# Kernel tuning notes

Measured on AMD Instinct MI355X. Metric: run time of the kernel, lower is better.

Reference implementation:

```python
import jax, jax.numpy as jnp
import numpy as np
import math

B, SQ, SKV = 8, 1024, 1024
D, H, DQ, DV = 1024, 16, 64, 64
EPS = 1e-3  # Keras LayerNormalization default epsilon
IN_DECODER = True


def _layer_norm(x, gamma, beta):
    m = jnp.mean(x, axis=-1, keepdims=True)
    v = jnp.mean((x - m) ** 2, axis=-1, keepdims=True)
    return gamma * (x - m) / jnp.sqrt(v + EPS) + beta


def setup_inputs() -> dict:
    key = jax.random.key(0)
    ks = jax.random.split(key, 6)
    x = jax.random.normal(ks[0], (B, SQ, D), dtype=jnp.float32)
    # self-attention: query and key/value sequences are the same tensor
    lengths = jax.random.randint(ks[1], (B,), SKV // 2, SKV + 1, dtype=jnp.int32)
    init = 0.02
    Wq = jax.random.normal(ks[2], (D, H * DQ), dtype=jnp.float32) * init
    Wkv = jax.random.normal(ks[3], (D, H * (DQ + DV)), dtype=jnp.float32) * init
    Wo = jax.random.normal(ks[4], (H * DV, D), dtype=jnp.float32) * init
    return {
        "query_sequences": x,
        "key_value_sequences": x,
        "key_value_sequence_lengths": lengths,
        "Wq": Wq, "bq": jnp.zeros((H * DQ,), jnp.float32),
        "Wkv": Wkv, "bkv": jnp.zeros((H * (DQ + DV),), jnp.float32),
        "Wo": Wo, "bo": jnp.zeros((D,), jnp.float32),
        "ln_gamma": jnp.ones((D,), jnp.float32),
        "ln_beta": jnp.zeros((D,), jnp.float32),
    }


def reference(query_sequences, key_value_sequences, key_value_sequence_lengths,
              Wq, bq, Wkv, bkv, Wo, bo, ln_gamma, ln_beta):
    # detect self-attention exactly as the original (elementwise equality)
    self_attn = jnp.all(query_sequences == key_value_sequences)
    q_seq = _layer_norm(query_sequences, ln_gamma, ln_beta)
    kv_ln = _layer_norm(key_value_sequences, ln_gamma, ln_beta)
    kv_seq = jnp.where(self_attn, kv_ln, key_value_sequences)
    residual = q_seq  # pre-norm residual (original adds post-LN queries)

    q = (q_seq @ Wq + bq).reshape(B, SQ, H, DQ).transpose(0, 2, 1, 3)   # b h q d
    kvp = kv_seq @ Wkv + bkv
    k = kvp[..., : H * DQ].reshape(B, SKV, H, DQ).transpose(0, 2, 1, 3)  # b h k d
    v = kvp[..., H * DQ:].reshape(B, SKV, H, DV).transpose(0, 2, 1, 3)   # b h k d

    scores = jnp.einsum("bhqd,bhkd->bhqk", q, k) / math.sqrt(DQ)
    # padding mask on keys
    not_pad = (jnp.arange(SKV)[None, None, None, :]
               < key_value_sequence_lengths[:, None, None, None])
    scores = jnp.where(not_pad, scores, -jnp.inf)
    if IN_DECODER:
        causal = jnp.tril(jnp.ones((SQ, SKV), dtype=bool))[None, None]
        scores = jnp.where(jnp.logical_or(~self_attn, causal), scores, -jnp.inf)

    attn = jax.nn.softmax(scores, axis=-1)  # dropout is identity in eval mode
    out = jnp.einsum("bhqk,bhkd->bhqd", attn, v)
    out = out.transpose(0, 2, 1, 3).reshape(B, SQ, H * DV)
    out = out @ Wo + bo
    return out + residual
```

## Files before the change

kernel.cpp:

```cpp
#include <hip/hip_runtime.h>

typedef unsigned short u16;
typedef unsigned int u32;
typedef __attribute__((ext_vector_type(8))) short short8;
typedef __attribute__((ext_vector_type(4))) float fx4;

#define LOG2E 1.44269504088896340736f

__device__ __forceinline__ u16 f2bf(float f) {
    unsigned int u = __float_as_uint(f);
    u += 0x7fffu + ((u >> 16) & 1u);
    return (u16)(u >> 16);
}

__device__ __forceinline__ float bf2f(u16 v) {
    u32 u = ((u32)v) << 16;
    return __uint_as_float(u);
}

__device__ __forceinline__ u32 pack_bf2(float lo, float hi) {
    return __builtin_amdgcn_perm(__float_as_uint(hi), __float_as_uint(lo), 0x07060302u);
}

__device__ __forceinline__ float fast_exp2(float x) {
#if __has_builtin(__builtin_amdgcn_exp2f)
    return __builtin_amdgcn_exp2f(x);
#else
    return exp2f(x);
#endif
}

__device__ __forceinline__ fx4 mfma16(short8 a, short8 b, fx4 c) {
    return __builtin_amdgcn_mfma_f32_16x16x32_bf16(a, b, c, 0, 0, 0);
}

__device__ __forceinline__ void gload_lds16(const u16* g, u16* l) {
    __builtin_amdgcn_global_load_lds(
        (const __attribute__((address_space(1))) void*)g,
        (__attribute__((address_space(3))) void*)l, 16, 0, 0);
}

__global__ __launch_bounds__(256) void ln_kernel(
    const float* __restrict__ x, const float* __restrict__ gamma,
    const float* __restrict__ beta, u16* __restrict__ yb) {
    int wave = threadIdx.x >> 6, lane = threadIdx.x & 63;
    int row = (blockIdx.x << 2) + wave;
    const float* xr = x + ((size_t)row << 10);
    float4 v[4];
    float s = 0.0f, sq = 0.0f;
#pragma unroll
    for (int i = 0; i < 4; ++i) {
        v[i] = *(const float4*)(xr + (i << 8) + (lane << 2));
        s  += v[i].x + v[i].y + v[i].z + v[i].w;
        sq += v[i].x * v[i].x + v[i].y * v[i].y + v[i].z * v[i].z + v[i].w * v[i].w;
    }
#pragma unroll
    for (int o = 32; o > 0; o >>= 1) {
        s  += __shfl_xor(s, o, 64);
        sq += __shfl_xor(sq, o, 64);
    }
    float mean = s * (1.0f / 1024.0f);
    float var  = sq * (1.0f / 1024.0f) - mean * mean;
    float rstd = rsqrtf(var + 1e-3f);
#pragma unroll
    for (int i = 0; i < 4; ++i) {
        int off = (i << 8) + (lane << 2);
        float4 g  = *(const float4*)(gamma + off);
        float4 bb = *(const float4*)(beta + off);
        float4 y;
        y.x = (v[i].x - mean) * rstd * g.x + bb.x;
        y.y = (v[i].y - mean) * rstd * g.y + bb.y;
        y.z = (v[i].z - mean) * rstd * g.z + bb.z;
        y.w = (v[i].w - mean) * rstd * g.w + bb.w;
        unsigned long long p = (unsigned long long)f2bf(y.x)
            | ((unsigned long long)f2bf(y.y) << 16)
            | ((unsigned long long)f2bf(y.z) << 32)
            | ((unsigned long long)f2bf(y.w) << 48);
        *(unsigned long long*)(yb + ((size_t)row << 10) + off) = p;
    }
}

__global__ __launch_bounds__(256) void wt_kernel(
    const float* __restrict__ Wq, const float* __restrict__ Wkv,
    const float* __restrict__ Wo, u16* __restrict__ Wt) {
    int n0 = blockIdx.x << 5;
    int k0 = blockIdx.y << 5;
    const float* W; int sn0, SN;
    if (n0 < 1024)      { W = Wq;  sn0 = n0;        SN = 1024; }
    else if (n0 < 3072) { W = Wkv; sn0 = n0 - 1024; SN = 2048; }
    else                { W = Wo;  sn0 = n0 - 3072; SN = 1024; }
    __shared__ float tile[32][33];
    int tx = threadIdx.x & 31, ty = threadIdx.x >> 5;
#pragma unroll
    for (int r = 0; r < 4; ++r)
        tile[ty + r * 8][tx] = W[(size_t)(k0 + ty + r * 8) * SN + sn0 + tx];
    __syncthreads();
#pragma unroll
    for (int r = 0; r < 4; ++r)
        Wt[(size_t)(n0 + ty + r * 8) * 1024 + k0 + tx] = f2bf(tile[tx][ty + r * 8]);
}

__global__ __launch_bounds__(256) void vtrans_kernel(
    const u16* __restrict__ QKVp, u16* __restrict__ Vt) {
    int bh = blockIdx.x;
    int b = bh >> 4, h = bh & 15;
    int kt = blockIdx.y;
    int t = threadIdx.x;
    __shared__ u16 tile[64][80];
    int seg = t & 7;
#pragma unroll
    for (int p = 0; p < 2; ++p) {
        int k = (t >> 3) + (p << 5);
        *(uint4*)&tile[k][seg << 3] =
            *(const uint4*)(QKVp + (size_t)((b << 10) + (kt << 6) + k) * 3072
                            + 2048 + (h << 6) + (seg << 3));
    }
    __syncthreads();
#pragma unroll
    for (int p = 0; p < 2; ++p) {
        int d = (t >> 3) + (p << 5);
        __align__(16) u16 vals[8];
#pragma unroll
        for (int e = 0; e < 8; ++e) {
            int kp = (seg << 3) + e;
            int ksrc = ((kp & 3) << 4) + (kp >> 2);
            vals[e] = tile[ksrc][d];
        }
        *(uint4*)(Vt + (size_t)((bh << 6) + d) * 1024 + (kt << 6) + (seg << 3)) =
            *(uint4*)vals;
    }
}

template <int MODE, int WMT>
__global__ __launch_bounds__(256) void gemm_bt(
    const u16* __restrict__ A, const u16* __restrict__ Bt,
    const float* __restrict__ bq, const float* __restrict__ bkv,
    const u16* __restrict__ resb, float* __restrict__ Cf, u16* __restrict__ Cb,
    int M, int N, int K, float qscale) {
    __shared__ __align__(16) u16 sA[WMT * 32 * 64];
    __shared__ __align__(16) u16 sB[128 * 64];
    int m0 = blockIdx.y * (WMT * 32), n0 = blockIdx.x << 7;
    int tid = threadIdx.x, lane = tid & 63, wave = tid >> 6;
    int quad = lane >> 4, l15 = lane & 15, swr = lane & 7;
    int wm = (wave >> 1) * (WMT * 16), wn = (wave & 1) << 6;
    int srow = lane >> 3;
    int gseg = (lane & 7) ^ srow;

    fx4 acc[WMT][4];
    fx4 zero = {0.0f, 0.0f, 0.0f, 0.0f};
#pragma unroll
    for (int i = 0; i < WMT; ++i)
#pragma unroll
        for (int j = 0; j < 4; ++j) acc[i][j] = zero;

    for (int k0 = 0; k0 < K; k0 += 64) {
#pragma unroll
        for (int t = 0; t < WMT; ++t) {
            int cA = wave * WMT + t;
            int rowA = (cA << 3) + srow;
            gload_lds16(A + (size_t)(m0 + rowA) * K + k0 + (gseg << 3), &sA[cA << 9]);
            if (t < 4) {
                int cB = (wave << 2) + t;
                int rowB = (cB << 3) + srow;
                gload_lds16(Bt + (size_t)(n0 + rowB) * K + k0 + (gseg << 3), &sB[cB << 9]);
            }
        }
        __syncthreads();
#pragma unroll
        for (int kk = 0; kk < 64; kk += 32) {
            int ks = (kk >> 3) + quad;
            short8 af[WMT], bf[4];
#pragma unroll
            for (int mt = 0; mt < WMT; ++mt) {
                int r = wm + (mt << 4) + l15;
                af[mt] = *(const short8*)&sA[(r << 6) + (((ks ^ swr) & 7) << 3)];
            }
#pragma unroll
            for (int nt = 0; nt < 4; ++nt) {
                int r = wn + (nt << 4) + l15;
                bf[nt] = *(const short8*)&sB[(r << 6) + (((ks ^ swr) & 7) << 3)];
            }
#pragma unroll
            for (int mt = 0; mt < WMT; ++mt)
#pragma unroll
                for (int nt = 0; nt < 4; ++nt)
                    acc[mt][nt] = mfma16(af[mt], bf[nt], acc[mt][nt]);
        }
        __syncthreads();
    }

#pragma unroll
    for (int mt = 0; mt < WMT; ++mt)
#pragma unroll
        for (int nt = 0; nt < 4; ++nt)
#pragma unroll
            for (int r = 0; r < 4; ++r) {
                int row = m0 + wm + (mt << 4) + (quad << 2) + r;
                int col = n0 + wn + (nt << 4) + l15;
                if (MODE == 1) {
                    float v = acc[mt][nt][r] + bq[col];
                    size_t idx = (size_t)row * N + col;
                    Cf[idx] = v + bf2f(resb[idx]);
                } else {
                    float bias = (col < 1024) ? bq[col] : bkv[col - 1024];
                    float v = acc[mt][nt][r] + bias;
                    if (col < 1024) v *= qscale;
                    Cb[(size_t)row * N + col] = f2bf(v);
                }
            }
}

__global__ __launch_bounds__(256) void attn_kernel(
    const u16* __restrict__ QKVp, const u16* __restrict__ Vt,
    const int* __restrict__ lens, u16* __restrict__ O) {
    int bh = blockIdx.x;
    int b = bh >> 4, h = bh & 15;
    int j = blockIdx.y;
    int len = lens[b];
    int cap = (len - 1) >> 6;
    int tid = threadIdx.x, lane = tid & 63, w = tid >> 6;
    int quad = lane >> 4, l15 = lane & 15;

    __shared__ __align__(16) u16 sK[64 * 64];
    __shared__ __align__(16) u16 sV[64 * 64];
    __shared__ __align__(16) u16 sP[4 * 2048];
    u16* sPw = &sP[w << 11];

    int lrow = lane >> 3;
    int lseg = lane & 7;

    fx4 zero = {0.0f, 0.0f, 0.0f, 0.0f};

#pragma unroll
    for (int phase = 0; phase < 2; ++phase) {
        int s = phase ? (7 - j) : j;
        int q0 = s << 7;
        int wq0 = q0 + (w << 5);
        int ktend_blk = min((q0 + 127) >> 6, cap);
        int ktend_w   = min((wq0 + 31) >> 6, cap);

        short8 qf[2][2];
#pragma unroll
        for (int mt = 0; mt < 2; ++mt)
#pragma unroll
            for (int kk = 0; kk < 2; ++kk) {
                int qrow = (b << 10) + wq0 + (mt << 4) + l15;
                qf[mt][kk] = *(const short8*)(QKVp + (size_t)qrow * 3072
                              + (h << 6) + (kk << 5) + (quad << 3));
            }

        fx4 oacc[2][4];
        float lsum[2][4];
#pragma unroll
        for (int mt = 0; mt < 2; ++mt)
#pragma unroll
            for (int nt = 0; nt < 4; ++nt) oacc[mt][nt] = zero;
#pragma unroll
        for (int mt = 0; mt < 2; ++mt)
#pragma unroll
            for (int r = 0; r < 4; ++r) lsum[mt][r] = 0.0f;

        for (int kt = 0; kt <= ktend_blk; ++kt) {
            int k0g = kt << 6;
#pragma unroll
            for (int i = 0; i < 2; ++i) {
                int row = (w << 4) + (i << 3) + lrow;
                int gs = lseg ^ (row & 7);
                gload_lds16(QKVp + (size_t)((b << 10) + k0g + row) * 3072
                               + 1024 + (h << 6) + (gs << 3),
                            &sK[((w << 1) + i) << 9]);
                gload_lds16(Vt + (size_t)((bh << 6) + row) * 1024
                               + k0g + (gs << 3),
                            &sV[((w << 1) + i) << 9]);
            }
            __syncthreads();

            if (kt <= ktend_w) {
                fx4 sacc[2][4];
#pragma unroll
                for (int mt = 0; mt < 2; ++mt)
#pragma unroll
                    for (int nt = 0; nt < 4; ++nt) sacc[mt][nt] = zero;
#pragma unroll
                for (int kk = 0; kk < 2; ++kk) {
                    int seg = (kk << 2) + quad;
                    short8 kf[4];
#pragma unroll
                    for (int nt = 0; nt < 4; ++nt) {
                        int row = (nt << 4) + l15;
                        kf[nt] = *(const short8*)&sK[(row << 6)
                                   + (((seg ^ (row & 7)) & 7) << 3)];
                    }
#pragma unroll
                    for (int mt = 0; mt < 2; ++mt)
#pragma unroll
                        for (int nt = 0; nt < 4; ++nt)
                            sacc[mt][nt] = mfma16(qf[mt][kk], kf[nt], sacc[mt][nt]);
                }

                bool needm = ((k0g + 63) > wq0) || ((k0g + 64) > len);
                if (needm) {
#pragma unroll
                    for (int mt = 0; mt < 2; ++mt)
#pragma unroll
                        for (int nt = 0; nt < 4; ++nt) {
                            int kg = k0g + (nt << 4) + l15;
#pragma unroll
                            for (int r = 0; r < 4; ++r) {
                                int qr = wq0 + (mt << 4) + (quad << 2) + r;
                                if (kg > qr || kg >= len)
                                    sacc[mt][nt][r] = -30000.0f;
                            }
                        }
                }

#pragma unroll
                for (int mt = 0; mt < 2; ++mt) {
#pragma unroll
                    for (int nt = 0; nt < 4; ++nt)
#pragma unroll
                        for (int r = 0; r < 4; ++r)
                            sacc[mt][nt][r] = fast_exp2(sacc[mt][nt][r]);
#pragma unroll
                    for (int r = 0; r < 4; ++r) {
                        lsum[mt][r] += (sacc[mt][0][r] + sacc[mt][1][r])
                                     + (sacc[mt][2][r] + sacc[mt][3][r]);
                        int row = (mt << 4) + (quad << 2) + r;
                        u32 lo = pack_bf2(sacc[mt][0][r], sacc[mt][1][r]);
                        u32 hi = pack_bf2(sacc[mt][2][r], sacc[mt][3][r]);
                        uint2 pv; pv.x = lo; pv.y = hi;
                        int addr = (row << 6)
                                 + (((((l15 >> 1)) ^ (row & 7)) & 7) << 3)
                                 + ((l15 & 1) << 2);
                        *(uint2*)&sPw[addr] = pv;
                    }
                }
                __builtin_amdgcn_s_waitcnt(0xC07F);

#pragma unroll
                for (int kk = 0; kk < 2; ++kk) {
                    int seg = (kk << 2) + quad;
                    short8 vf[4], pf[2];
#pragma unroll
                    for (int nt = 0; nt < 4; ++nt) {
                        int row = (nt << 4) + l15;
                        vf[nt] = *(const short8*)&sV[(row << 6)
                                   + (((seg ^ (row & 7)) & 7) << 3)];
                    }
#pragma unroll
                    for (int mt = 0; mt < 2; ++mt) {
                        int row = (mt << 4) + l15;
                        pf[mt] = *(const short8*)&sPw[(row << 6)
                                   + (((seg ^ (row & 7)) & 7) << 3)];
                    }
#pragma unroll
                    for (int mt = 0; mt < 2; ++mt)
#pragma unroll
                        for (int nt = 0; nt < 4; ++nt)
                            oacc[mt][nt] = mfma16(pf[mt], vf[nt], oacc[mt][nt]);
                }
            }
            __syncthreads();
        }

#pragma unroll
        for (int mt = 0; mt < 2; ++mt)
#pragma unroll
            for (int r = 0; r < 4; ++r) {
                float v = lsum[mt][r];
                v += __shfl_xor(v, 1, 64);
                v += __shfl_xor(v, 2, 64);
                v += __shfl_xor(v, 4, 64);
                v += __shfl_xor(v, 8, 64);
                lsum[mt][r] = __builtin_amdgcn_rcpf(v);
            }
#pragma unroll
        for (int mt = 0; mt < 2; ++mt)
#pragma unroll
            for (int nt = 0; nt < 4; ++nt)
#pragma unroll
                for (int r = 0; r < 4; ++r) {
                    int row = (b << 10) + wq0 + (mt << 4) + (quad << 2) + r;
                    int col = (h << 6) + (nt << 4) + l15;
                    O[((size_t)row << 10) + col] =
                        f2bf(oacc[mt][nt][r] * lsum[mt][r]);
                }
    }
}

extern "C" void kernel_launch(void* const* d_in, const int* in_sizes, int n_in,
                              void* d_out, int out_size, void* d_ws, size_t ws_size,
                              hipStream_t stream) {
    (void)in_sizes; (void)n_in; (void)out_size; (void)ws_size;
    const float* x    = (const float*)d_in[0];
    const int*   lens = (const int*)d_in[2];
    const float* Wq   = (const float*)d_in[3];
    const float* bq   = (const float*)d_in[4];
    const float* Wkv  = (const float*)d_in[5];
    const float* bkv  = (const float*)d_in[6];
    const float* Wo   = (const float*)d_in[7];
    const float* bo   = (const float*)d_in[8];
    const float* gam  = (const float*)d_in[9];
    const float* bet  = (const float*)d_in[10];
    float* out = (float*)d_out;

    char* w = (char*)d_ws;
    u16* xln_b  = (u16*)w;  w += (size_t)8192 * 1024 * 2;
    u16* Wall_t = (u16*)w;  w += (size_t)4096 * 1024 * 2;
    u16* QKVp   = (u16*)w;  w += (size_t)8192 * 3072 * 2;
    u16* Vt     = (u16*)w;  w += (size_t)8192 * 1024 * 2;
    u16* AO     = (u16*)w;  w += (size_t)8192 * 1024 * 2;

    ln_kernel<<<2048, 256, 0, stream>>>(x, gam, bet, xln_b);
    wt_kernel<<<dim3(128, 32), 256, 0, stream>>>(Wq, Wkv, Wo, Wall_t);
    gemm_bt<0, 8><<<dim3(24, 32), 256, 0, stream>>>(xln_b, Wall_t, bq, bkv,
        nullptr, nullptr, QKVp, 8192, 3072, 1024, 0.125f * LOG2E);
    vtrans_kernel<<<dim3(128, 16), 256, 0, stream>>>(QKVp, Vt);
    attn_kernel<<<dim3(128, 4), 256, 0, stream>>>(QKVp, Vt, lens, AO);
    gemm_bt<1, 8><<<dim3(8, 32), 256, 0, stream>>>(AO, Wall_t + (size_t)3072 * 1024,
        bo, nullptr, xln_b, out, nullptr, 8192, 1024, 1024, 1.0f);
}
```

Measured before the change: 302.5 us.

## Fuse LN with weight transpose, write V transposed from QKV GEMM epilogue

Merges the layernorm and weight-transpose kernels into a single launch, split by block index. The QKV GEMM epilogue now writes the V columns straight into the permuted transposed Vt layout, which removes the separate vtrans kernel and its read-back of V. Both GEMMs also drop from 8 to 4 M-tiles per wave, doubling the grid for better occupancy at the cost of less reuse per block. The epilogue stores to Vt are scattered 2-byte writes, which may be poorly coalesced.

```diff
diff --git a/kernel.cpp b/kernel.cpp
--- a/kernel.cpp
+++ b/kernel.cpp
@@ -40,94 +40,65 @@
         (__attribute__((address_space(3))) void*)l, 16, 0, 0);
 }
 
-__global__ __launch_bounds__(256) void ln_kernel(
+__global__ __launch_bounds__(256) void ln_wt_kernel(
     const float* __restrict__ x, const float* __restrict__ gamma,
-    const float* __restrict__ beta, u16* __restrict__ yb) {
-    int wave = threadIdx.x >> 6, lane = threadIdx.x & 63;
-    int row = (blockIdx.x << 2) + wave;
-    const float* xr = x + ((size_t)row << 10);
-    float4 v[4];
-    float s = 0.0f, sq = 0.0f;
-#pragma unroll
-    for (int i = 0; i < 4; ++i) {
-        v[i] = *(const float4*)(xr + (i << 8) + (lane << 2));
-        s  += v[i].x + v[i].y + v[i].z + v[i].w;
-        sq += v[i].x * v[i].x + v[i].y * v[i].y + v[i].z * v[i].z + v[i].w * v[i].w;
-    }
-#pragma unroll
-    for (int o = 32; o > 0; o >>= 1) {
-        s  += __shfl_xor(s, o, 64);
-        sq += __shfl_xor(sq, o, 64);
-    }
-    float mean = s * (1.0f / 1024.0f);
-    float var  = sq * (1.0f / 1024.0f) - mean * mean;
-    float rstd = rsqrtf(var + 1e-3f);
-#pragma unroll
-    for (int i = 0; i < 4; ++i) {
-        int off = (i << 8) + (lane << 2);
-        float4 g  = *(const float4*)(gamma + off);
-        float4 bb = *(const float4*)(beta + off);
-        float4 y;
-        y.x = (v[i].x - mean) * rstd * g.x + bb.x;
-        y.y = (v[i].y - mean) * rstd * g.y + bb.y;
-        y.z = (v[i].z - mean) * rstd * g.z + bb.z;
-        y.w = (v[i].w - mean) * rstd * g.w + bb.w;
-        unsigned long long p = (unsigned long long)f2bf(y.x)
-            | ((unsigned long long)f2bf(y.y) << 16)
-            | ((unsigned long long)f2bf(y.z) << 32)
-            | ((unsigned long long)f2bf(y.w) << 48);
-        *(unsigned long long*)(yb + ((size_t)row << 10) + off) = p;
-    }
-}
-
-__global__ __launch_bounds__(256) void wt_kernel(
+    const float* __restrict__ beta, u16* __restrict__ yb,
     const float* __restrict__ Wq, const float* __restrict__ Wkv,
     const float* __restrict__ Wo, u16* __restrict__ Wt) {
-    int n0 = blockIdx.x << 5;
-    int k0 = blockIdx.y << 5;
-    const float* W; int sn0, SN;
-    if (n0 < 1024)      { W = Wq;  sn0 = n0;        SN = 1024; }
-    else if (n0 < 3072) { W = Wkv; sn0 = n0 - 1024; SN = 2048; }
-    else                { W = Wo;  sn0 = n0 - 3072; SN = 1024; }
-    __shared__ float tile[32][33];
-    int tx = threadIdx.x & 31, ty = threadIdx.x >> 5;
-#pragma unroll
-    for (int r = 0; r < 4; ++r)
-        tile[ty + r * 8][tx] = W[(size_t)(k0 + ty + r * 8) * SN + sn0 + tx];
-    __syncthreads();
-#pragma unroll
-    for (int r = 0; r < 4; ++r)
-        Wt[(size_t)(n0 + ty + r * 8) * 1024 + k0 + tx] = f2bf(tile[tx][ty + r * 8]);
-}
-
-__global__ __launch_bounds__(256) void vtrans_kernel(
-    const u16* __restrict__ QKVp, u16* __restrict__ Vt) {
-    int bh = blockIdx.x;
-    int b = bh >> 4, h = bh & 15;
-    int kt = blockIdx.y;
-    int t = threadIdx.x;
-    __shared__ u16 tile[64][80];
-    int seg = t & 7;
-#pragma unroll
-    for (int p = 0; p < 2; ++p) {
-        int k = (t >> 3) + (p << 5);
-        *(uint4*)&tile[k][seg << 3] =
-            *(const uint4*)(QKVp + (size_t)((b << 10) + (kt << 6) + k) * 3072
-                            + 2048 + (h << 6) + (seg << 3));
-    }
-    __syncthreads();
-#pragma unroll
-    for (int p = 0; p < 2; ++p) {
-        int d = (t >> 3) + (p << 5);
-        __align__(16) u16 vals[8];
-#pragma unroll
-        for (int e = 0; e < 8; ++e) {
-            int kp = (seg << 3) + e;
-            int ksrc = ((kp & 3) << 4) + (kp >> 2);
-            vals[e] = tile[ksrc][d];
-        }
-        *(uint4*)(Vt + (size_t)((bh << 6) + d) * 1024 + (kt << 6) + (seg << 3)) =
-            *(uint4*)vals;
+    int blk = blockIdx.x;
+    if (blk < 2048) {
+        int wave = threadIdx.x >> 6, lane = threadIdx.x & 63;
+        int row = (blk << 2) + wave;
+        const float* xr = x + ((size_t)row << 10);
+        float4 v[4];
+        float s = 0.0f, sq = 0.0f;
+#pragma unroll
+        for (int i = 0; i < 4; ++i) {
+            v[i] = *(const float4*)(xr + (i << 8) + (lane << 2));
+            s  += v[i].x + v[i].y + v[i].z + v[i].w;
+            sq += v[i].x * v[i].x + v[i].y * v[i].y + v[i].z * v[i].z + v[i].w * v[i].w;
+        }
+#pragma unroll
+        for (int o = 32; o > 0; o >>= 1) {
+            s  += __shfl_xor(s, o, 64);
+            sq += __shfl_xor(sq, o, 64);
+        }
+        float mean = s * (1.0f / 1024.0f);
+        float var  = sq * (1.0f / 1024.0f) - mean * mean;
+        float rstd = rsqrtf(var + 1e-3f);
+#pragma unroll
+        for (int i = 0; i < 4; ++i) {
+            int off = (i << 8) + (lane << 2);
+            float4 g  = *(const float4*)(gamma + off);
+            float4 bb = *(const float4*)(beta + off);
+            float4 y;
+            y.x = (v[i].x - mean) * rstd * g.x + bb.x;
+            y.y = (v[i].y - mean) * rstd * g.y + bb.y;
+            y.z = (v[i].z - mean) * rstd * g.z + bb.z;
+            y.w = (v[i].w - mean) * rstd * g.w + bb.w;
+            unsigned long long p = (unsigned long long)f2bf(y.x)
+                | ((unsigned long long)f2bf(y.y) << 16)
+                | ((unsigned long long)f2bf(y.z) << 32)
+                | ((unsigned long long)f2bf(y.w) << 48);
+            *(unsigned long long*)(yb + ((size_t)row << 10) + off) = p;
+        }
+    } else {
+        int wtb = blk - 2048;
+        int n0 = (wtb & 127) << 5;
+        int k0 = (wtb >> 7) << 5;
+        const float* W; int sn0, SN;
+        if (n0 < 1024)      { W = Wq;  sn0 = n0;        SN = 1024; }
+        else if (n0 < 3072) { W = Wkv; sn0 = n0 - 1024; SN = 2048; }
+        else                { W = Wo;  sn0 = n0 - 3072; SN = 1024; }
+        __shared__ float tile[32][33];
+        int tx = threadIdx.x & 31, ty = threadIdx.x >> 5;
+#pragma unroll
+        for (int r = 0; r < 4; ++r)
+            tile[ty + r * 8][tx] = W[(size_t)(k0 + ty + r * 8) * SN + sn0 + tx];
+        __syncthreads();
+#pragma unroll
+        for (int r = 0; r < 4; ++r)
+            Wt[(size_t)(n0 + ty + r * 8) * 1024 + k0 + tx] = f2bf(tile[tx][ty + r * 8]);
     }
 }
 
@@ -136,7 +107,7 @@
     const u16* __restrict__ A, const u16* __restrict__ Bt,
     const float* __restrict__ bq, const float* __restrict__ bkv,
     const u16* __restrict__ resb, float* __restrict__ Cf, u16* __restrict__ Cb,
-    int M, int N, int K, float qscale) {
+    u16* __restrict__ Vt, int M, int N, int K, float qscale) {
     __shared__ __align__(16) u16 sA[WMT * 32 * 64];
     __shared__ __align__(16) u16 sB[128 * 64];
     int m0 = blockIdx.y * (WMT * 32), n0 = blockIdx.x << 7;
@@ -187,6 +158,26 @@
                     acc[mt][nt] = mfma16(af[mt], bf[nt], acc[mt][nt]);
         }
         __syncthreads();
+    }
+
+    if (MODE == 0 && n0 >= 2048) {
+#pragma unroll
+        for (int mt = 0; mt < WMT; ++mt)
+#pragma unroll
+            for (int nt = 0; nt < 4; ++nt)
+#pragma unroll
+                for (int r = 0; r < 4; ++r) {
+                    int row = m0 + wm + (mt << 4) + (quad << 2) + r;
+                    int col = n0 + wn + (nt << 4) + l15;
+                    float v = acc[mt][nt][r] + bkv[col - 1024];
+                    int bb = row >> 10, k = row & 1023;
+                    int h = (col - 2048) >> 6, d = col & 63;
+                    int kt = k >> 6, kin = k & 63;
+                    int kp = ((kin & 15) << 2) | (kin >> 4);
+                    Vt[(size_t)((((bb << 4) + h) << 6) + d) * 1024
+                       + (kt << 6) + kp] = f2bf(v);
+                }
+        return;
     }
 
 #pragma unroll
@@ -411,12 +402,10 @@
     u16* Vt     = (u16*)w;  w += (size_t)8192 * 1024 * 2;
     u16* AO     = (u16*)w;  w += (size_t)8192 * 1024 * 2;
 
-    ln_kernel<<<2048, 256, 0, stream>>>(x, gam, bet, xln_b);
-    wt_kernel<<<dim3(128, 32), 256, 0, stream>>>(Wq, Wkv, Wo, Wall_t);
-    gemm_bt<0, 8><<<dim3(24, 32), 256, 0, stream>>>(xln_b, Wall_t, bq, bkv,
-        nullptr, nullptr, QKVp, 8192, 3072, 1024, 0.125f * LOG2E);
-    vtrans_kernel<<<dim3(128, 16), 256, 0, stream>>>(QKVp, Vt);
+    ln_wt_kernel<<<6144, 256, 0, stream>>>(x, gam, bet, xln_b, Wq, Wkv, Wo, Wall_t);
+    gemm_bt<0, 4><<<dim3(24, 64), 256, 0, stream>>>(xln_b, Wall_t, bq, bkv,
+        nullptr, nullptr, QKVp, Vt, 8192, 3072, 1024, 0.125f * LOG2E);
     attn_kernel<<<dim3(128, 4), 256, 0, stream>>>(QKVp, Vt, lens, AO);
-    gemm_bt<1, 8><<<dim3(8, 32), 256, 0, stream>>>(AO, Wall_t + (size_t)3072 * 1024,
-        bo, nullptr, xln_b, out, nullptr, 8192, 1024, 1024, 1.0f);
-}
+    gemm_bt<1, 4><<<dim3(8, 64), 256, 0, stream>>>(AO, Wall_t + (size_t)3072 * 1024,
+        bo, nullptr, xln_b, out, nullptr, nullptr, 8192, 1024, 1024, 1.0f);
+}
```

Measured after the change: 262.5 us. -13.2%, faster.
